# Kernel optimization log

Measured on AMD Instinct MI355X. Metric: run time of the kernel, lower is better.

## Reference

```python
import jax, jax.numpy as jnp
import numpy as np

N_NODES = 100000
N_EDGES = 600000
D_FEAT = 128
EDIM = 128
N_CLASSES = 10


def setup_inputs() -> dict:
    key = jax.random.key(0)
    k_h, k_eh, k_w, k_b, k_s, k_d = jax.random.split(key, 6)
    h = jax.random.normal(k_h, (N_NODES, D_FEAT), dtype=jnp.float32)
    edge_h = jax.random.normal(k_eh, (N_EDGES, 1, EDIM), dtype=jnp.float32)
    # Linear(in_features*2 + edim -> out_classes); torch stores weight as [out, in]
    W_w = jax.random.normal(k_w, (N_CLASSES, 2 * D_FEAT + EDIM), dtype=jnp.float32) * 0.05
    W_b = jax.random.normal(k_b, (N_CLASSES,), dtype=jnp.float32) * 0.05
    src = jax.random.randint(k_s, (N_EDGES,), 0, N_NODES, dtype=jnp.int64)
    dst = jax.random.randint(k_d, (N_EDGES,), 0, N_NODES, dtype=jnp.int64)
    return {"h": h, "edge_h": edge_h, "W_w": W_w, "W_b": W_b, "src": src, "dst": dst}


def reference(h, edge_h, W_w, W_b, src, dst):
    # edge-wise gather of src/dst node features
    h_u = h[src]                      # [E, D]
    h_v = h[dst]                      # [E, D]
    h_uv = edge_h.reshape(edge_h.shape[0], edge_h.shape[2])  # [E, edim]
    feat = jnp.concatenate([h_u, h_v, h_uv], axis=1)          # [E, 2D+edim]
    score = feat @ W_w.T + W_b                                 # [E, C]
    return score
```

## Files before the change

### kernel.cpp

```cpp
#include <hip/hip_runtime.h>


typedef __attribute__((ext_vector_type(8))) short short8;
typedef __attribute__((ext_vector_type(4))) float f32x4;

#define NC    10
#define TPW   4
#define NFRAG 12
#define FRAG_BYTES 12288
#define PSTRIDE 16

__device__ __forceinline__ unsigned short f2bf(float f) {
    unsigned u = __builtin_bit_cast(unsigned, f);
    u += 0x7FFFu + ((u >> 16) & 1u);
    return (unsigned short)(u >> 16);
}

__device__ __forceinline__ short8 cvt8(f32x4 a, f32x4 b) {
    short8 s;
    s[0]=(short)f2bf(a[0]); s[1]=(short)f2bf(a[1]);
    s[2]=(short)f2bf(a[2]); s[3]=(short)f2bf(a[3]);
    s[4]=(short)f2bf(b[0]); s[5]=(short)f2bf(b[1]);
    s[6]=(short)f2bf(b[2]); s[7]=(short)f2bf(b[3]);
    return s;
}

__global__ void build_wfrag(const float* __restrict__ Ww, short8* __restrict__ frag) {
    const int l = threadIdx.x;
    const int n = l & 15;
    const int q = l >> 4;
#pragma unroll
    for (int t = 0; t < NFRAG; ++t) {
        short8 b = (short8)0;
        if (n < NC) {
            const float* w = Ww + n * 384 + t * 32 + q * 8;
            b = cvt8(*(const f32x4*)w, *(const f32x4*)(w + 4));
        }
        frag[t * 64 + l] = b;
    }
}

#define LGF(v0,v1,v2,v3,v4,v5,v6,v7,p)          \
    v0 = *(const f32x4*)((p) + 0);              \
    v1 = *(const f32x4*)((p) + 4);              \
    v2 = *(const f32x4*)((p) + 32);             \
    v3 = *(const f32x4*)((p) + 36);             \
    v4 = *(const f32x4*)((p) + 64);             \
    v5 = *(const f32x4*)((p) + 68);             \
    v6 = *(const f32x4*)((p) + 96);             \
    v7 = *(const f32x4*)((p) + 100);

__global__ __launch_bounds__(64) void build_ptab(
    const float* __restrict__ h, const short8* __restrict__ frag,
    const float* __restrict__ Wb, float* __restrict__ P1,
    float* __restrict__ P2, int N)
{
    const int l = threadIdx.x;
    const int n = l & 15;
    const int q = l >> 4;
    short8 bf[8];
#pragma unroll
    for (int t = 0; t < 8; ++t) bf[t] = frag[t * 64 + l];
    const float bias = (n < NC) ? Wb[n] : 0.f;

    const long base = (long)blockIdx.x * 16;
    const long node = base + n;
    const long ndc = (node < N) ? node : (long)(N - 1);
    const float* ph = h + ndc * 128 + q * 8;

    f32x4 x0,x1,x2,x3,x4,x5,x6,x7;
    LGF(x0,x1,x2,x3,x4,x5,x6,x7, ph)
    const short8 a0 = cvt8(x0,x1), a1 = cvt8(x2,x3);
    const short8 a2 = cvt8(x4,x5), a3 = cvt8(x6,x7);

    f32x4 acc1 = {0.f,0.f,0.f,0.f}, acc2 = {0.f,0.f,0.f,0.f};
    acc1 = __builtin_amdgcn_mfma_f32_16x16x32_bf16(a0, bf[0], acc1, 0,0,0);
    acc1 = __builtin_amdgcn_mfma_f32_16x16x32_bf16(a1, bf[1], acc1, 0,0,0);
    acc1 = __builtin_amdgcn_mfma_f32_16x16x32_bf16(a2, bf[2], acc1, 0,0,0);
    acc1 = __builtin_amdgcn_mfma_f32_16x16x32_bf16(a3, bf[3], acc1, 0,0,0);
    acc2 = __builtin_amdgcn_mfma_f32_16x16x32_bf16(a0, bf[4], acc2, 0,0,0);
    acc2 = __builtin_amdgcn_mfma_f32_16x16x32_bf16(a1, bf[5], acc2, 0,0,0);
    acc2 = __builtin_amdgcn_mfma_f32_16x16x32_bf16(a2, bf[6], acc2, 0,0,0);
    acc2 = __builtin_amdgcn_mfma_f32_16x16x32_bf16(a3, bf[7], acc2, 0,0,0);

#pragma unroll
    for (int r = 0; r < 4; ++r) {
        const long nd = base + q * 4 + r;
        if (nd < N) {
            P1[nd * PSTRIDE + n] = acc1[r] + bias;
            P2[nd * PSTRIDE + n] = acc2[r];
        }
    }
}

__global__ __launch_bounds__(64, 4) void mlp_edge_fused(
    const float* __restrict__ eh,
    const short8* __restrict__ frag,
    const float* __restrict__ P1,
    const float* __restrict__ P2,
    const int*   __restrict__ src,
    const int*   __restrict__ dst,
    float* __restrict__ out,
    int E)
{
    const int l = threadIdx.x;
    const int n = l & 15;
    const int q = l >> 4;

    const short8 bf0 = frag[ 8 * 64 + l];
    const short8 bf1 = frag[ 9 * 64 + l];
    const short8 bf2 = frag[10 * 64 + l];
    const short8 bf3 = frag[11 * 64 + l];
    const int cn = (n < NC) ? n : 0;

    const long tile0 = (long)blockIdx.x * TPW;

#pragma unroll 1
    for (int tt = 0; tt < TPW; ++tt) {
        const long base = (tile0 + tt) * 16;
        if (base >= E) break;
        const long e  = base + n;
        const long ec = (e < E) ? e : (long)(E - 1);
        const float* pe = eh + ec * 128 + q * 8;

        f32x4 z0,z1,z2,z3,z4,z5,z6,z7;
        LGF(z0,z1,z2,z3,z4,z5,z6,z7, pe)

        int s2[4], d2[4];
#pragma unroll
        for (int r = 0; r < 4; ++r) {
            const long e2  = base + q * 4 + r;
            const long e2c = (e2 < E) ? e2 : (long)(E - 1);
            s2[r] = src[e2c];
            d2[r] = dst[e2c];
        }
        float pv1[4], pv2[4];
#pragma unroll
        for (int r = 0; r < 4; ++r) {
            pv1[r] = P1[(long)s2[r] * PSTRIDE + cn];
            pv2[r] = P2[(long)d2[r] * PSTRIDE + cn];
        }

        f32x4 acc = {0.f, 0.f, 0.f, 0.f};
        acc = __builtin_amdgcn_mfma_f32_16x16x32_bf16(cvt8(z0,z1), bf0, acc, 0,0,0);
        acc = __builtin_amdgcn_mfma_f32_16x16x32_bf16(cvt8(z2,z3), bf1, acc, 0,0,0);
        acc = __builtin_amdgcn_mfma_f32_16x16x32_bf16(cvt8(z4,z5), bf2, acc, 0,0,0);
        acc = __builtin_amdgcn_mfma_f32_16x16x32_bf16(cvt8(z6,z7), bf3, acc, 0,0,0);

        if (n < NC) {
#pragma unroll
            for (int r = 0; r < 4; ++r) {
                const long e2 = base + q * 4 + r;
                if (e2 < E) out[e2 * NC + n] = acc[r] + pv1[r] + pv2[r];
            }
        }
    }
}

__global__ __launch_bounds__(64, 3) void mlp_edge_f32(
    const float* __restrict__ h, const float* __restrict__ eh,
    const short8* __restrict__ frag, const float* __restrict__ Wb,
    const int* __restrict__ src, const int* __restrict__ dst,
    float* __restrict__ out, int E)
{
    const int l = threadIdx.x;
    const int n = l & 15;
    const int q = l >> 4;

    short8 bf[NFRAG];
#pragma unroll
    for (int t = 0; t < NFRAG; ++t) bf[t] = frag[t * 64 + l];
    const float bias = (n < NC) ? Wb[n] : 0.f;

    const long tile0 = (long)blockIdx.x * TPW;

#pragma unroll 1
    for (int tt = 0; tt < TPW; ++tt) {
        const long base = (tile0 + tt) * 16;
        if (base >= E) break;
        const long e  = base + n;
        const long ec = (e < E) ? e : (long)(E - 1);
        const int  sA = src[ec];
        const int  dA = dst[ec];
        const float* pe = eh + ec * 128 + q * 8;
        const float* ps = h + (long)sA * 128 + q * 8;
        const float* pd = h + (long)dA * 128 + q * 8;

        f32x4 x0,x1,x2,x3,x4,x5,x6,x7;
        f32x4 y0,y1,y2,y3,y4,y5,y6,y7;
        f32x4 z0,z1,z2,z3,z4,z5,z6,z7;
        LGF(x0,x1,x2,x3,x4,x5,x6,x7, ps)
        LGF(y0,y1,y2,y3,y4,y5,y6,y7, pd)
        LGF(z0,z1,z2,z3,z4,z5,z6,z7, pe)

        f32x4 acc = {0.f, 0.f, 0.f, 0.f};
        acc = __builtin_amdgcn_mfma_f32_16x16x32_bf16(cvt8(x0,x1), bf[0], acc, 0,0,0);
        acc = __builtin_amdgcn_mfma_f32_16x16x32_bf16(cvt8(x2,x3), bf[1], acc, 0,0,0);
        acc = __builtin_amdgcn_mfma_f32_16x16x32_bf16(cvt8(x4,x5), bf[2], acc, 0,0,0);
        acc = __builtin_amdgcn_mfma_f32_16x16x32_bf16(cvt8(x6,x7), bf[3], acc, 0,0,0);
        acc = __builtin_amdgcn_mfma_f32_16x16x32_bf16(cvt8(y0,y1), bf[4], acc, 0,0,0);
        acc = __builtin_amdgcn_mfma_f32_16x16x32_bf16(cvt8(y2,y3), bf[5], acc, 0,0,0);
        acc = __builtin_amdgcn_mfma_f32_16x16x32_bf16(cvt8(y4,y5), bf[6], acc, 0,0,0);
        acc = __builtin_amdgcn_mfma_f32_16x16x32_bf16(cvt8(y6,y7), bf[7], acc, 0,0,0);
        acc = __builtin_amdgcn_mfma_f32_16x16x32_bf16(cvt8(z0,z1), bf[8],  acc, 0,0,0);
        acc = __builtin_amdgcn_mfma_f32_16x16x32_bf16(cvt8(z2,z3), bf[9],  acc, 0,0,0);
        acc = __builtin_amdgcn_mfma_f32_16x16x32_bf16(cvt8(z4,z5), bf[10], acc, 0,0,0);
        acc = __builtin_amdgcn_mfma_f32_16x16x32_bf16(cvt8(z6,z7), bf[11], acc, 0,0,0);

        if (n < NC) {
#pragma unroll
            for (int r = 0; r < 4; ++r) {
                const long e2 = base + q * 4 + r;
                if (e2 < E) out[e2 * NC + n] = acc[r] + bias;
            }
        }
    }
}

extern "C" void kernel_launch(void* const* d_in, const int* in_sizes, int n_in,
                              void* d_out, int out_size, void* d_ws, size_t ws_size,
                              hipStream_t stream) {
    const float* h   = (const float*)d_in[0];
    const float* eh  = (const float*)d_in[1];
    const float* Ww  = (const float*)d_in[2];
    const float* Wb  = (const float*)d_in[3];
    const int*   src = (const int*)d_in[4];
    const int*   dst = (const int*)d_in[5];
    float* out = (float*)d_out;

    const int E    = in_sizes[4];
    const int N128 = in_sizes[0];
    const int N    = N128 / 128;

    short8* frag = (short8*)d_ws;
    build_wfrag<<<1, 64, 0, stream>>>(Ww, frag);

    const int edgesPerBlock = 16 * TPW;
    const int blocks = (E + edgesPerBlock - 1) / edgesPerBlock;

    const size_t pfloats = (size_t)N * PSTRIDE;
    const size_t need = (size_t)FRAG_BYTES + 2 * pfloats * sizeof(float);
    if (ws_size >= need) {
        float* P1 = (float*)((char*)d_ws + FRAG_BYTES);
        float* P2 = P1 + pfloats;
        build_ptab<<<(N + 15) / 16, 64, 0, stream>>>(h, frag, Wb, P1, P2, N);
        mlp_edge_fused<<<blocks, 64, 0, stream>>>(eh, frag, P1, P2, src, dst, out, E);
    } else {
        mlp_edge_f32<<<blocks, 64, 0, stream>>>(h, eh, frag, Wb, src, dst, out, E);
    }
}
```

Measured before the change: 459.5 us.

## Drop weight-fragment prep kernel and widen blocks to four waves

Removes the separate build_wfrag launch, so each wave now builds its bf16 weight fragments directly from Ww in registers. build_ptab and mlp_edge_fused move from 64-thread to 256-thread blocks, each wave handling its own tile range, which cuts the block count by four. 64-bit index arithmetic is narrowed to 32-bit with size_t casts only where offsets can overflow. The goal is one fewer kernel launch and lower per-block overhead, at the cost of redundant fp32-to-bf16 weight conversion in every wave.

```diff
diff --git a/kernel.cpp b/kernel.cpp
--- a/kernel.cpp
+++ b/kernel.cpp
@@ -4,10 +4,8 @@
 typedef __attribute__((ext_vector_type(8))) short short8;
 typedef __attribute__((ext_vector_type(4))) float f32x4;
 
-#define NC    10
-#define TPW   4
-#define NFRAG 12
-#define FRAG_BYTES 12288
+#define NC      10
+#define TPW     4
 #define PSTRIDE 16
 
 __device__ __forceinline__ unsigned short f2bf(float f) {
@@ -25,19 +23,14 @@
     return s;
 }
 
-__global__ void build_wfrag(const float* __restrict__ Ww, short8* __restrict__ frag) {
-    const int l = threadIdx.x;
-    const int n = l & 15;
-    const int q = l >> 4;
-#pragma unroll
-    for (int t = 0; t < NFRAG; ++t) {
-        short8 b = (short8)0;
-        if (n < NC) {
-            const float* w = Ww + n * 384 + t * 32 + q * 8;
-            b = cvt8(*(const f32x4*)w, *(const f32x4*)(w + 4));
-        }
-        frag[t * 64 + l] = b;
-    }
+__device__ __forceinline__ short8 wfrag(const float* __restrict__ Ww,
+                                        int t, int n, int q) {
+    short8 b = (short8)0;
+    if (n < NC) {
+        const float* w = Ww + n * 384 + t * 32 + q * 8;
+        b = cvt8(*(const f32x4*)w, *(const f32x4*)(w + 4));
+    }
+    return b;
 }
 
 #define LGF(v0,v1,v2,v3,v4,v5,v6,v7,p)          \
@@ -50,22 +43,24 @@
     v6 = *(const f32x4*)((p) + 96);             \
     v7 = *(const f32x4*)((p) + 100);
 
-__global__ __launch_bounds__(64) void build_ptab(
-    const float* __restrict__ h, const short8* __restrict__ frag,
+__global__ __launch_bounds__(256) void build_ptab(
+    const float* __restrict__ h, const float* __restrict__ Ww,
     const float* __restrict__ Wb, float* __restrict__ P1,
     float* __restrict__ P2, int N)
 {
-    const int l = threadIdx.x;
+    const int l = threadIdx.x & 63;
+    const int w = threadIdx.x >> 6;
     const int n = l & 15;
     const int q = l >> 4;
+
     short8 bf[8];
 #pragma unroll
-    for (int t = 0; t < 8; ++t) bf[t] = frag[t * 64 + l];
+    for (int t = 0; t < 8; ++t) bf[t] = wfrag(Ww, t, n, q);
     const float bias = (n < NC) ? Wb[n] : 0.f;
 
-    const long base = (long)blockIdx.x * 16;
-    const long node = base + n;
-    const long ndc = (node < N) ? node : (long)(N - 1);
+    const int base = blockIdx.x * 64 + w * 16;
+    const int node = base + n;
+    const int ndc = (node < N) ? node : (N - 1);
     const float* ph = h + ndc * 128 + q * 8;
 
     f32x4 x0,x1,x2,x3,x4,x5,x6,x7;
@@ -85,7 +80,7 @@
 
 #pragma unroll
     for (int r = 0; r < 4; ++r) {
-        const long nd = base + q * 4 + r;
+        const int nd = base + q * 4 + r;
         if (nd < N) {
             P1[nd * PSTRIDE + n] = acc1[r] + bias;
             P2[nd * PSTRIDE + n] = acc2[r];
@@ -93,9 +88,9 @@
     }
 }
 
-__global__ __launch_bounds__(64, 4) void mlp_edge_fused(
+__global__ __launch_bounds__(256, 4) void mlp_edge_fused(
     const float* __restrict__ eh,
-    const short8* __restrict__ frag,
+    const float* __restrict__ Ww,
     const float* __restrict__ P1,
     const float* __restrict__ P2,
     const int*   __restrict__ src,
@@ -103,25 +98,26 @@
     float* __restrict__ out,
     int E)
 {
-    const int l = threadIdx.x;
+    const int l = threadIdx.x & 63;
+    const int w = threadIdx.x >> 6;
     const int n = l & 15;
     const int q = l >> 4;
 
-    const short8 bf0 = frag[ 8 * 64 + l];
-    const short8 bf1 = frag[ 9 * 64 + l];
-    const short8 bf2 = frag[10 * 64 + l];
-    const short8 bf3 = frag[11 * 64 + l];
+    const short8 bf0 = wfrag(Ww,  8, n, q);
+    const short8 bf1 = wfrag(Ww,  9, n, q);
+    const short8 bf2 = wfrag(Ww, 10, n, q);
+    const short8 bf3 = wfrag(Ww, 11, n, q);
     const int cn = (n < NC) ? n : 0;
 
-    const long tile0 = (long)blockIdx.x * TPW;
+    const int tile0 = blockIdx.x * 16 + w * TPW;
 
 #pragma unroll 1
     for (int tt = 0; tt < TPW; ++tt) {
-        const long base = (tile0 + tt) * 16;
+        const int base = (tile0 + tt) * 16;
         if (base >= E) break;
-        const long e  = base + n;
-        const long ec = (e < E) ? e : (long)(E - 1);
-        const float* pe = eh + ec * 128 + q * 8;
+        const int e  = base + n;
+        const int ec = (e < E) ? e : (E - 1);
+        const float* pe = eh + (size_t)ec * 128 + q * 8;
 
         f32x4 z0,z1,z2,z3,z4,z5,z6,z7;
         LGF(z0,z1,z2,z3,z4,z5,z6,z7, pe)
@@ -129,16 +125,16 @@
         int s2[4], d2[4];
 #pragma unroll
         for (int r = 0; r < 4; ++r) {
-            const long e2  = base + q * 4 + r;
-            const long e2c = (e2 < E) ? e2 : (long)(E - 1);
+            const int e2  = base + q * 4 + r;
+            const int e2c = (e2 < E) ? e2 : (E - 1);
             s2[r] = src[e2c];
             d2[r] = dst[e2c];
         }
         float pv1[4], pv2[4];
 #pragma unroll
         for (int r = 0; r < 4; ++r) {
-            pv1[r] = P1[(long)s2[r] * PSTRIDE + cn];
-            pv2[r] = P2[(long)d2[r] * PSTRIDE + cn];
+            pv1[r] = P1[s2[r] * PSTRIDE + cn];
+            pv2[r] = P2[d2[r] * PSTRIDE + cn];
         }
 
         f32x4 acc = {0.f, 0.f, 0.f, 0.f};
@@ -150,8 +146,8 @@
         if (n < NC) {
 #pragma unroll
             for (int r = 0; r < 4; ++r) {
-                const long e2 = base + q * 4 + r;
-                if (e2 < E) out[e2 * NC + n] = acc[r] + pv1[r] + pv2[r];
+                const int e2 = base + q * 4 + r;
+                if (e2 < E) out[(size_t)e2 * NC + n] = acc[r] + pv1[r] + pv2[r];
             }
         }
     }
@@ -159,7 +155,7 @@
 
 __global__ __launch_bounds__(64, 3) void mlp_edge_f32(
     const float* __restrict__ h, const float* __restrict__ eh,
-    const short8* __restrict__ frag, const float* __restrict__ Wb,
+    const float* __restrict__ Ww, const float* __restrict__ Wb,
     const int* __restrict__ src, const int* __restrict__ dst,
     float* __restrict__ out, int E)
 {
@@ -167,24 +163,24 @@
     const int n = l & 15;
     const int q = l >> 4;
 
-    short8 bf[NFRAG];
-#pragma unroll
-    for (int t = 0; t < NFRAG; ++t) bf[t] = frag[t * 64 + l];
+    short8 bf[12];
+#pragma unroll
+    for (int t = 0; t < 12; ++t) bf[t] = wfrag(Ww, t, n, q);
     const float bias = (n < NC) ? Wb[n] : 0.f;
 
-    const long tile0 = (long)blockIdx.x * TPW;
+    const int tile0 = blockIdx.x * TPW;
 
 #pragma unroll 1
     for (int tt = 0; tt < TPW; ++tt) {
-        const long base = (tile0 + tt) * 16;
+        const int base = (tile0 + tt) * 16;
         if (base >= E) break;
-        const long e  = base + n;
-        const long ec = (e < E) ? e : (long)(E - 1);
+        const int e  = base + n;
+        const int ec = (e < E) ? e : (E - 1);
         const int  sA = src[ec];
         const int  dA = dst[ec];
-        const float* pe = eh + ec * 128 + q * 8;
-        const float* ps = h + (long)sA * 128 + q * 8;
-        const float* pd = h + (long)dA * 128 + q * 8;
+        const float* pe = eh + (size_t)ec * 128 + q * 8;
+        const float* ps = h + (size_t)sA * 128 + q * 8;
+        const float* pd = h + (size_t)dA * 128 + q * 8;
 
         f32x4 x0,x1,x2,x3,x4,x5,x6,x7;
         f32x4 y0,y1,y2,y3,y4,y5,y6,y7;
@@ -210,8 +206,8 @@
         if (n < NC) {
 #pragma unroll
             for (int r = 0; r < 4; ++r) {
-                const long e2 = base + q * 4 + r;
-                if (e2 < E) out[e2 * NC + n] = acc[r] + bias;
+                const int e2 = base + q * 4 + r;
+                if (e2 < E) out[(size_t)e2 * NC + n] = acc[r] + bias;
             }
         }
     }
@@ -232,20 +228,17 @@
     const int N128 = in_sizes[0];
     const int N    = N128 / 128;
 
-    short8* frag = (short8*)d_ws;
-    build_wfrag<<<1, 64, 0, stream>>>(Ww, frag);
-
-    const int edgesPerBlock = 16 * TPW;
-    const int blocks = (E + edgesPerBlock - 1) / edgesPerBlock;
-
     const size_t pfloats = (size_t)N * PSTRIDE;
-    const size_t need = (size_t)FRAG_BYTES + 2 * pfloats * sizeof(float);
+    const size_t need = 2 * pfloats * sizeof(float);
+
     if (ws_size >= need) {
-        float* P1 = (float*)((char*)d_ws + FRAG_BYTES);
+        float* P1 = (float*)d_ws;
         float* P2 = P1 + pfloats;
-        build_ptab<<<(N + 15) / 16, 64, 0, stream>>>(h, frag, Wb, P1, P2, N);
-        mlp_edge_fused<<<blocks, 64, 0, stream>>>(eh, frag, P1, P2, src, dst, out, E);
+        build_ptab<<<(N + 63) / 64, 256, 0, stream>>>(h, Ww, Wb, P1, P2, N);
+        const int blocks = (E + 255) / 256;
+        mlp_edge_fused<<<blocks, 256, 0, stream>>>(eh, Ww, P1, P2, src, dst, out, E);
     } else {
-        mlp_edge_f32<<<blocks, 64, 0, stream>>>(h, eh, frag, Wb, src, dst, out, E);
-    }
-}
+        const int blocks = (E + 16 * TPW - 1) / (16 * TPW);
+        mlp_edge_f32<<<blocks, 64, 0, stream>>>(h, eh, Ww, Wb, src, dst, out, E);
+    }
+}
```

Measured after the change: 468.5 us. No clear change (+2.0%).
